# Kernel optimization log

Measured on AMD Instinct MI355X. Metric: run time of the kernel, lower is better.

## Reference

```python
import jax, jax.numpy as jnp
import numpy as np

# Fixed multi-scale geometry implied by the module's hard-coded reshapes
# (48^2=2304, 24^2=576, 12^2=144; Len_q = 576).
SPATIAL = [(48, 48), (24, 24), (12, 12)]
NH, NP, NL = 6, 4, 3  # num_heads, num_points, num_levels


def _process_reference_points(rp):
    """rp: (B, 3024, 2) normalized refs over 3 levels -> (B, 576, 2).
    Mirrors the part1/part2/part3 averaging in MSDeformAttn.forward."""
    B = rp.shape[0]
    p1 = rp[:, :2304].reshape(B, 48, 48, 2).mean(axis=(1, 2))[:, None, :]
    p1 = jnp.broadcast_to(p1, (B, 576, 2))
    p2 = rp[:, 2304:2880].reshape(B, 576, 2)
    p3 = rp[:, 2880:].reshape(B, 12, 12, 2)
    p3 = jax.image.resize(p3, (B, 24, 24, 2), 'bilinear')  # align_corners=False
    p3 = p3.reshape(B, 576, 2)
    return (p1 + p2 + p3) / 3.0


def _bilinear_sample(val_l, coords, Hl, Wl):
    """val_l: (B, Hl*Wl, nh, d) one level's values.
    coords: (B, Lq, nh, P, 2) normalized (x, y) sampling locations.
    Returns (B, Lq, P, nh, d) bilinearly sampled values (zero padding)."""
    B, Lq, nh, P, _ = coords.shape
    px = coords[..., 0] * Wl - 0.5
    py = coords[..., 1] * Hl - 0.5
    x0 = jnp.floor(px)
    y0 = jnp.floor(py)
    lx = px - x0
    ly = py - y0
    x0i = x0.astype(jnp.int32)
    y0i = y0.astype(jnp.int32)

    def _flat(a):  # (B,Lq,nh,P) -> (B,Lq*P,nh,1) matching value layout
        return a.transpose(0, 1, 3, 2).reshape(B, Lq * P, nh, 1)

    def gather(xi, yi):
        valid = (xi >= 0) & (xi < Wl) & (yi >= 0) & (yi < Hl)
        xi_c = jnp.clip(xi, 0, Wl - 1)
        yi_c = jnp.clip(yi, 0, Hl - 1)
        idx = _flat(yi_c * Wl + xi_c)
        v = jnp.take_along_axis(val_l, idx, axis=1)  # (B,Lq*P,nh,d)
        return v * _flat(valid).astype(val_l.dtype)

    w00 = _flat((1 - lx) * (1 - ly))
    w10 = _flat(lx * (1 - ly))
    w01 = _flat((1 - lx) * ly)
    w11 = _flat(lx * ly)
    out = (gather(x0i, y0i) * w00 + gather(x0i + 1, y0i) * w10 +
           gather(x0i, y0i + 1) * w01 + gather(x0i + 1, y0i + 1) * w11)
    return out.reshape(B, Lq, P, nh, -1)


def setup_inputs() -> dict:
    key = jax.random.key(0)
    ks = jax.random.split(key, 8)
    B, C = 32, 384
    Lq, Lv = 576, 3024
    # reference points exactly as get_reference_points builds them
    refs = []
    for (Hl, Wl) in SPATIAL:
        ry, rx = np.meshgrid(np.linspace(0.5, Hl - 0.5, Hl) / Hl,
                             np.linspace(0.5, Wl - 0.5, Wl) / Wl, indexing='ij')
        refs.append(np.stack([rx.ravel(), ry.ravel()], -1))
    rp = np.concatenate(refs, 0).astype(np.float32)  # (3024, 2)
    rp = np.broadcast_to(rp[None, :, None, :], (B, Lv, 1, 2)).copy()
    s = 1.0 / np.sqrt(C)
    return {
        'query': jax.random.normal(ks[0], (B, Lq, C), jnp.float32),
        'value': jax.random.normal(ks[1], (B, Lv, C), jnp.float32),
        'reference_points': jnp.asarray(rp),
        'W_value': jax.random.normal(ks[2], (C, C), jnp.float32) * s,
        'b_value': jnp.zeros((C,), jnp.float32),
        'W_off': jax.random.normal(ks[3], (C, NH * NL * NP * 2), jnp.float32) * 0.01,
        'b_off': jnp.zeros((NH * NL * NP * 2,), jnp.float32),
        'W_attn': jax.random.normal(ks[4], (C, NH * NL * NP), jnp.float32) * s,
        'b_attn': jnp.zeros((NH * NL * NP,), jnp.float32),
        'W_out': jax.random.normal(ks[5], (C, C), jnp.float32) * s,
        'b_out': jnp.zeros((C,), jnp.float32),
    }


def reference(query, value, reference_points, W_value, b_value, W_off, b_off,
              W_attn, b_attn, W_out, b_out):
    B, Lq, C = query.shape
    d = C // NH
    val = (value @ W_value + b_value).reshape(B, -1, NH, d)
    off = (query @ W_off + b_off).reshape(B, Lq, NH, NL, NP, 2)
    attn = jax.nn.softmax((query @ W_attn + b_attn)
                          .reshape(B, Lq, NH, NL * NP), axis=-1)
    attn = attn.reshape(B, Lq, NH, NL, NP)
    ref = _process_reference_points(reference_points.reshape(B, -1, 2))
    coords = off + ref[:, :, None, None, None, :]  # (B,Lq,nh,L,P,2)
    out = jnp.zeros((B, Lq, NH, d), query.dtype)
    start = 0
    for l, (Hl, Wl) in enumerate(SPATIAL):
        val_l = val[:, start:start + Hl * Wl]
        sampled = _bilinear_sample(val_l, coords[:, :, :, l], Hl, Wl)
        out = out + jnp.einsum('bqpnd,bqnp->bqnd', sampled, attn[:, :, :, l])
        start += Hl * Wl
    return out.reshape(B, Lq, NH * d) @ W_out + b_out
```

## Files before the change

kernel.cpp:

```cpp
#include <hip/hip_runtime.h>
#include <cmath>

#define B_SZ   32
#define LQ     576
#define LV     3024
#define CDIM   384
#define NHEAD  6
#define DHEAD  64
#define NLVL   3
#define NPTS   4
#define NPROJ  216
#define NPROJP 256

typedef short    bx4 __attribute__((ext_vector_type(4)));
typedef short    bx8 __attribute__((ext_vector_type(8)));
typedef float    fx4 __attribute__((ext_vector_type(4)));
typedef _Float16 hx8 __attribute__((ext_vector_type(8)));

__device__ __forceinline__ short f2bf(float f) {
    unsigned u = __builtin_bit_cast(unsigned, f);
    unsigned r = (u + 0x7FFFu + ((u >> 16) & 1u)) >> 16;
    return (short)r;
}
__device__ __forceinline__ float bf2f(unsigned short u) {
    return __builtin_bit_cast(float, ((unsigned)u) << 16);
}
__device__ __forceinline__ short f2h(float f) {
    return __builtin_bit_cast(short, (_Float16)f);
}

__global__ __launch_bounds__(256) void cast_transpose_kernel(
    const float* __restrict__ W, short* __restrict__ Wt, int K, int N)
{
    int idx = blockIdx.x * 256 + threadIdx.x;
    if (idx >= K * N) return;
    int n = idx / K, k = idx - n * K;
    Wt[idx] = f2bf(W[(size_t)k * N + n]);
}

__global__ __launch_bounds__(256) void prep_proj_f16_kernel(
    const float* __restrict__ W_off, const float* __restrict__ b_off,
    const float* __restrict__ W_attn, const float* __restrict__ b_attn,
    short* __restrict__ Wf, float* __restrict__ bc)
{
    int idx = blockIdx.x * 256 + threadIdx.x;
    if (idx >= NPROJP * CDIM) return;
    int n = idx / CDIM, k = idx - n * CDIM;
    float w = 0.f;
    if (n < 144)           w = W_off[(size_t)k * 144 + n];
    else if (n < NPROJ)    w = W_attn[(size_t)k * 72 + (n - 144)];
    Wf[idx] = f2h(w);
    if (idx < NPROJP)
        bc[idx] = (idx < 144) ? b_off[idx]
                 : (idx < NPROJ ? b_attn[idx - 144] : 0.f);
}

__global__ __launch_bounds__(512) void value_gemm_kernel(
    const float* __restrict__ A, const short* __restrict__ Bt,
    const float* __restrict__ bias, short* __restrict__ Cout,
    int M, int K)
{
    constexpr int N = 384;
    __shared__ short As[128 * 64];
    __shared__ short Bs[384 * 64];

    const int tid = threadIdx.x;
    const int m0 = blockIdx.x * 128;

    const int w  = tid >> 6;
    const int l  = tid & 63;
    const int wr = (w & 1) * 64;
    const int wc = (w >> 1) * 96;
    const int lr = l & 15;
    const int q  = l >> 4;

    const int rg  = l >> 3;
    const int cg  = l & 7;
    const int csw = cg ^ rg;

    const int am = tid >> 2;
    const int ak = (tid & 3) << 4;

    fx4 acc[4][6] = {};

    for (int k0 = 0; k0 < K; k0 += 64) {
        #pragma unroll
        for (int t = 0; t < 6; ++t) {
            const int rbase = w * 48 + t * 8;
            const short* gB = Bt + (size_t)(rbase + rg) * K + k0 + csw * 8;
            __builtin_amdgcn_global_load_lds(
                (const __attribute__((address_space(1))) void*)gB,
                (__attribute__((address_space(3))) void*)&Bs[rbase * 64],
                16, 0, 0);
        }
        {
            const float* gA = A + (size_t)(m0 + am) * K + k0 + ak;
            const float4 v0 = *(const float4*)(gA + 0);
            const float4 v1 = *(const float4*)(gA + 4);
            const float4 v2 = *(const float4*)(gA + 8);
            const float4 v3 = *(const float4*)(gA + 12);
            bx8 s0, s1;
            s0[0] = f2bf(v0.x); s0[1] = f2bf(v0.y); s0[2] = f2bf(v0.z); s0[3] = f2bf(v0.w);
            s0[4] = f2bf(v1.x); s0[5] = f2bf(v1.y); s0[6] = f2bf(v1.z); s0[7] = f2bf(v1.w);
            s1[0] = f2bf(v2.x); s1[1] = f2bf(v2.y); s1[2] = f2bf(v2.z); s1[3] = f2bf(v2.w);
            s1[4] = f2bf(v3.x); s1[5] = f2bf(v3.y); s1[6] = f2bf(v3.z); s1[7] = f2bf(v3.w);
            const int ob = ak >> 3;
            const int o0 = (ob + 0) ^ (am & 7);
            const int o1 = (ob + 1) ^ (am & 7);
            *(bx8*)&As[am * 64 + o0 * 8] = s0;
            *(bx8*)&As[am * 64 + o1 * 8] = s1;
        }
        __syncthreads();

        #pragma unroll
        for (int ks = 0; ks < 2; ++ks) {
            bx8 af[4], bf[6];
            #pragma unroll
            for (int i = 0; i < 4; ++i)
                af[i] = *(const bx8*)&As[(wr + i * 16 + lr) * 64 +
                                         (((ks * 4 + q) ^ (lr & 7)) << 3)];
            #pragma unroll
            for (int j = 0; j < 6; ++j)
                bf[j] = *(const bx8*)&Bs[(wc + j * 16 + lr) * 64 +
                                         (((ks * 4 + q) ^ (lr & 7)) << 3)];
            #pragma unroll
            for (int i = 0; i < 4; ++i)
                #pragma unroll
                for (int j = 0; j < 6; ++j)
                    acc[i][j] = __builtin_amdgcn_mfma_f32_16x16x32_bf16(
                        af[i], bf[j], acc[i][j], 0, 0, 0);
        }
        __syncthreads();
    }

    const int rrow = q * 4;
    #pragma unroll
    for (int j = 0; j < 6; ++j) {
        const int col = wc + j * 16 + lr;
        const float bv = bias[col];
        #pragma unroll
        for (int i = 0; i < 4; ++i) {
            const int row = m0 + wr + i * 16 + rrow;
            #pragma unroll
            for (int r = 0; r < 4; ++r)
                Cout[(size_t)(row + r) * N + col] = f2bf(acc[i][j][r] + bv);
        }
    }
}

template <bool OUT_BF16>
__global__ __launch_bounds__(256) void gemm_dma_kernel(
    const short* __restrict__ A, const short* __restrict__ Bt,
    const float* __restrict__ bias, void* __restrict__ Cout,
    int M, int K)
{
    constexpr int N = 384;
    __shared__ short As[128 * 64];
    __shared__ short Bs[128 * 64];

    const int tid = threadIdx.x;
    const int n0 = blockIdx.x * 128;
    const int m0 = blockIdx.y * 128;

    const int w  = tid >> 6;
    const int l  = tid & 63;
    const int wr = (w & 1) * 64;
    const int wc = (w >> 1) * 64;
    const int lr = l & 15;
    const int q  = l >> 4;

    const int rg  = l >> 3;
    const int cg  = l & 7;
    const int csw = cg ^ rg;

    fx4 acc[4][4] = {};

    for (int k0 = 0; k0 < K; k0 += 64) {
        #pragma unroll
        for (int t = 0; t < 4; ++t) {
            const int rbase = w * 32 + t * 8;
            const short* gA = A + (size_t)(m0 + rbase + rg) * K + k0 + csw * 8;
            __builtin_amdgcn_global_load_lds(
                (const __attribute__((address_space(1))) void*)gA,
                (__attribute__((address_space(3))) void*)&As[rbase * 64],
                16, 0, 0);
            const short* gB = Bt + (size_t)(n0 + rbase + rg) * K + k0 + csw * 8;
            __builtin_amdgcn_global_load_lds(
                (const __attribute__((address_space(1))) void*)gB,
                (__attribute__((address_space(3))) void*)&Bs[rbase * 64],
                16, 0, 0);
        }
        __syncthreads();

        #pragma unroll
        for (int ks = 0; ks < 2; ++ks) {
            bx8 af[4], bf[4];
            #pragma unroll
            for (int i = 0; i < 4; ++i)
                af[i] = *(const bx8*)&As[(wr + i * 16 + lr) * 64 +
                                         (((ks * 4 + q) ^ (lr & 7)) << 3)];
            #pragma unroll
            for (int j = 0; j < 4; ++j)
                bf[j] = *(const bx8*)&Bs[(wc + j * 16 + lr) * 64 +
                                         (((ks * 4 + q) ^ (lr & 7)) << 3)];
            #pragma unroll
            for (int i = 0; i < 4; ++i)
                #pragma unroll
                for (int j = 0; j < 4; ++j)
                    acc[i][j] = __builtin_amdgcn_mfma_f32_16x16x32_bf16(
                        af[i], bf[j], acc[i][j], 0, 0, 0);
        }
        __syncthreads();
    }

    const int rrow = q * 4;
    #pragma unroll
    for (int j = 0; j < 4; ++j) {
        const int col = n0 + wc + j * 16 + lr;
        const float bv = bias[col];
        #pragma unroll
        for (int i = 0; i < 4; ++i) {
            const int row = m0 + wr + i * 16 + rrow;
            #pragma unroll
            for (int r = 0; r < 4; ++r) {
                if (OUT_BF16)
                    ((short*)Cout)[(size_t)(row + r) * N + col] = f2bf(acc[i][j][r] + bv);
                else
                    ((float*)Cout)[(size_t)(row + r) * N + col] = acc[i][j][r] + bv;
            }
        }
    }
}

__global__ __launch_bounds__(256) void gemm_proj_kernel(
    const float* __restrict__ A, const short* __restrict__ Wf,
    const float* __restrict__ bias, float* __restrict__ C,
    int M, int K)
{
    __shared__ short As[128 * 72];
    __shared__ short Bs[128 * 72];

    const int tid = threadIdx.x;
    const int n0 = blockIdx.x * 128;
    const int m0 = blockIdx.y * 128;

    const int w  = tid >> 6;
    const int l  = tid & 63;
    const int wr = (w & 1) * 64;
    const int wc = (w >> 1) * 64;
    const int lr = l & 15;
    const int ko = (l >> 4) * 8;

    fx4 acc[4][4] = {};

    for (int k0 = 0; k0 < K; k0 += 64) {
        #pragma unroll
        for (int r = 0; r < 8; ++r) {
            const int id = tid + r * 256;
            const int m  = id >> 4;
            const int kq = (id & 15) << 2;
            const float4 v = *(const float4*)(A + (size_t)(m0 + m) * K + k0 + kq);
            bx4 s;
            s[0] = f2h(v.x); s[1] = f2h(v.y); s[2] = f2h(v.z); s[3] = f2h(v.w);
            *(bx4*)&As[m * 72 + kq] = s;
        }
        #pragma unroll
        for (int r = 0; r < 4; ++r) {
            const int id = tid + r * 256;
            const int n  = id >> 3;
            const int k8 = (id & 7) << 3;
            *(bx8*)&Bs[n * 72 + k8] = *(const bx8*)(Wf + (size_t)(n0 + n) * K + k0 + k8);
        }
        __syncthreads();

        #pragma unroll
        for (int ks = 0; ks < 2; ++ks) {
            bx8 af[4], bf[4];
            #pragma unroll
            for (int i = 0; i < 4; ++i)
                af[i] = *(const bx8*)&As[(wr + i * 16 + lr) * 72 + ks * 32 + ko];
            #pragma unroll
            for (int j = 0; j < 4; ++j)
                bf[j] = *(const bx8*)&Bs[(wc + j * 16 + lr) * 72 + ks * 32 + ko];
            #pragma unroll
            for (int i = 0; i < 4; ++i)
                #pragma unroll
                for (int j = 0; j < 4; ++j)
                    acc[i][j] = __builtin_amdgcn_mfma_f32_16x16x32_f16(
                        __builtin_bit_cast(hx8, af[i]),
                        __builtin_bit_cast(hx8, bf[j]), acc[i][j], 0, 0, 0);
        }
        __syncthreads();
    }

    const int rrow = (l >> 4) * 4;
    #pragma unroll
    for (int j = 0; j < 4; ++j) {
        const int col = n0 + wc + j * 16 + lr;
        if (col >= NPROJ) continue;
        const float bv = bias[col];
        #pragma unroll
        for (int i = 0; i < 4; ++i) {
            const int row = m0 + wr + i * 16 + rrow;
            #pragma unroll
            for (int r = 0; r < 4; ++r)
                C[(size_t)(row + r) * NPROJ + col] = acc[i][j][r] + bv;
        }
    }
}

__global__ __launch_bounds__(256) void ref_kernel(
    const float* __restrict__ rp, float* __restrict__ refp)
{
    const int b = blockIdx.x;
    const float* r = rp + (size_t)b * LV * 2;
    const int tid = threadIdx.x;

    __shared__ float redx[256], redy[256];
    float sx = 0.f, sy = 0.f;
    for (int i = tid; i < 2304; i += 256) {
        sx += r[2 * i + 0];
        sy += r[2 * i + 1];
    }
    redx[tid] = sx; redy[tid] = sy;
    __syncthreads();
    for (int s = 128; s > 0; s >>= 1) {
        if (tid < s) { redx[tid] += redx[tid + s]; redy[tid] += redy[tid + s]; }
        __syncthreads();
    }
    const float p1x = redx[0] * (1.f / 2304.f);
    const float p1y = redy[0] * (1.f / 2304.f);

    const float* g = r + 2880 * 2;
    for (int q = tid; q < 576; q += 256) {
        const float p2x = r[(2304 + q) * 2 + 0];
        const float p2y = r[(2304 + q) * 2 + 1];
        const int qy = q / 24, qx = q % 24;
        const float syc = fminf(fmaxf(0.5f * qy - 0.25f, 0.f), 11.f);
        const float sxc = fminf(fmaxf(0.5f * qx - 0.25f, 0.f), 11.f);
        int y0 = min((int)syc, 10);
        int x0 = min((int)sxc, 10);
        const float fy = syc - (float)y0, fx = sxc - (float)x0;
        const float v00x = g[(y0 * 12 + x0) * 2 + 0],     v00y = g[(y0 * 12 + x0) * 2 + 1];
        const float v10x = g[(y0 * 12 + x0 + 1) * 2 + 0], v10y = g[(y0 * 12 + x0 + 1) * 2 + 1];
        const float v01x = g[((y0 + 1) * 12 + x0) * 2 + 0],     v01y = g[((y0 + 1) * 12 + x0) * 2 + 1];
        const float v11x = g[((y0 + 1) * 12 + x0 + 1) * 2 + 0], v11y = g[((y0 + 1) * 12 + x0 + 1) * 2 + 1];
        const float p3x = (1.f - fy) * ((1.f - fx) * v00x + fx * v10x)
                        + fy * ((1.f - fx) * v01x + fx * v11x);
        const float p3y = (1.f - fy) * ((1.f - fx) * v00y + fx * v10y)
                        + fy * ((1.f - fx) * v01y + fx * v11y);
        refp[((size_t)b * LQ + q) * 2 + 0] = (p1x + p2x + p3x) * (1.f / 3.f);
        refp[((size_t)b * LQ + q) * 2 + 1] = (p1y + p2y + p3y) * (1.f / 3.f);
    }
}

__global__ __launch_bounds__(192) void sample_kernel(
    const unsigned short* __restrict__ val, const float* __restrict__ proj,
    const float* __restrict__ refp, unsigned* __restrict__ mid)
{
    const int i = blockIdx.x;
    const int g = i & 7;
    const int r = i >> 3;
    const int b = g * 4 + (r / LQ);
    const int q = r - (r / LQ) * LQ;
    const int bq = b * LQ + q;
    const int tid = threadIdx.x;

    __shared__ float attn[72];
    __shared__ int   sloc[72][4];
    __shared__ float swt[72][4];

    if (tid < 72) {
        attn[tid] = proj[(size_t)bq * NPROJ + 144 + tid];

        const int h = tid / 12;
        const int rr = tid % 12;
        const int l = rr >> 2;
        const int p = rr & 3;

        const int HL[3] = {48, 24, 12};
        const int ST[3] = {0, 2304, 2880};
        const int Hl = HL[l], Wl = HL[l], st = ST[l];

        const float rx = refp[bq * 2 + 0];
        const float ry = refp[bq * 2 + 1];
        const int oc = ((h * NLVL + l) * NPTS + p) * 2;
        const float cx = proj[(size_t)bq * NPROJ + oc + 0] + rx;
        const float cy = proj[(size_t)bq * NPROJ + oc + 1] + ry;

        const float px = cx * (float)Wl - 0.5f;
        const float py = cy * (float)Hl - 0.5f;
        const float x0f = floorf(px), y0f = floorf(py);
        const float lx = px - x0f, ly = py - y0f;
        const int x0 = (int)x0f, y0 = (int)y0f;

        #pragma unroll
        for (int k = 0; k < 4; ++k) {
            const int dx = k & 1, dy = k >> 1;
            const int xi = x0 + dx, yi = y0 + dy;
            const bool v = (xi >= 0) && (xi < Wl) && (yi >= 0) && (yi < Hl);
            const int xc = min(max(xi, 0), Wl - 1);
            const int yc = min(max(yi, 0), Hl - 1);
            sloc[tid][k] = st + yc * Wl + xc;
            const float wx = dx ? lx : 1.f - lx;
            const float wy = dy ? ly : 1.f - ly;
            swt[tid][k] = v ? wx * wy : 0.f;
        }
    }
    __syncthreads();

    if (tid < NHEAD) {
        float mx = -1e30f;
        #pragma unroll
        for (int j = 0; j < 12; ++j) mx = fmaxf(mx, attn[tid * 12 + j]);
        float s = 0.f;
        #pragma unroll
        for (int j = 0; j < 12; ++j) {
            const float e = expf(attn[tid * 12 + j] - mx);
            attn[tid * 12 + j] = e;
            s += e;
        }
        const float inv = 1.f / s;
        #pragma unroll
        for (int j = 0; j < 12; ++j) attn[tid * 12 + j] *= inv;
    }
    __syncthreads();

    const int h  = tid >> 5;
    const int c2 = (tid & 31) << 1;
    const unsigned* vp = (const unsigned*)(val + (size_t)b * LV * CDIM + h * DHEAD + c2);
    float acc0 = 0.f, acc1 = 0.f;
    #pragma unroll
    for (int s = 0; s < 12; ++s) {
        const int j = h * 12 + s;
        const float a = attn[j];
        float s0 = 0.f, s1 = 0.f;
        #pragma unroll
        for (int k = 0; k < 4; ++k) {
            const unsigned u = vp[(size_t)sloc[j][k] * (CDIM / 2)];
            const float lo = __builtin_bit_cast(float, u << 16);
            const float hi = __builtin_bit_cast(float, u & 0xFFFF0000u);
            s0 += swt[j][k] * lo;
            s1 += swt[j][k] * hi;
        }
        acc0 += a * s0;
        acc1 += a * s1;
    }
    const unsigned lo = (unsigned)(unsigned short)f2bf(acc0);
    const unsigned hi = (unsigned)(unsigned short)f2bf(acc1);
    mid[((size_t)bq * CDIM + h * DHEAD + c2) >> 1] = lo | (hi << 16);
}

extern "C" void kernel_launch(void* const* d_in, const int* in_sizes, int n_in,
                              void* d_out, int out_size, void* d_ws, size_t ws_size,
                              hipStream_t stream)
{
    (void)in_sizes; (void)n_in; (void)out_size; (void)ws_size;

    const float* query   = (const float*)d_in[0];
    const float* value   = (const float*)d_in[1];
    const float* rp      = (const float*)d_in[2];
    const float* W_value = (const float*)d_in[3];
    const float* b_value = (const float*)d_in[4];
    const float* W_off   = (const float*)d_in[5];
    const float* b_off   = (const float*)d_in[6];
    const float* W_attn  = (const float*)d_in[7];
    const float* b_attn  = (const float*)d_in[8];
    const float* W_out   = (const float*)d_in[9];
    const float* b_out   = (const float*)d_in[10];
    float* out = (float*)d_out;

    char* p = (char*)d_ws;
    auto take = [&](size_t bytes) { char* q = p; p += (bytes + 255) & ~(size_t)255; return q; };
    short* val  = (short*)take((size_t)B_SZ * LV * CDIM * 2);
    short* mid  = (short*)take((size_t)B_SZ * LQ * CDIM * 2);
    short* Wtv  = (short*)take((size_t)CDIM * CDIM * 2);
    short* Wto  = (short*)take((size_t)CDIM * CDIM * 2);
    short* Wf   = (short*)take((size_t)NPROJP * CDIM * 2);
    float* proj = (float*)take((size_t)B_SZ * LQ * NPROJ * 4);
    float* refp = (float*)take((size_t)B_SZ * LQ * 2 * 4);
    float* bc   = (float*)take((size_t)NPROJP * 4);

    const int Mv = B_SZ * LV;
    const int Mq = B_SZ * LQ;

    cast_transpose_kernel<<<(CDIM * CDIM + 255) / 256, 256, 0, stream>>>(
        W_value, Wtv, CDIM, CDIM);
    cast_transpose_kernel<<<(CDIM * CDIM + 255) / 256, 256, 0, stream>>>(
        W_out, Wto, CDIM, CDIM);
    prep_proj_f16_kernel<<<(NPROJP * CDIM + 255) / 256, 256, 0, stream>>>(
        W_off, b_off, W_attn, b_attn, Wf, bc);

    value_gemm_kernel<<<Mv / 128, 512, 0, stream>>>(
        value, Wtv, b_value, val, Mv, CDIM);
    gemm_proj_kernel<<<dim3(2, Mq / 128), 256, 0, stream>>>(
        query, Wf, bc, proj, Mq, CDIM);
    ref_kernel<<<B_SZ, 256, 0, stream>>>(rp, refp);
    sample_kernel<<<Mq, 192, 0, stream>>>(
        (const unsigned short*)val, proj, refp, (unsigned*)mid);
    gemm_dma_kernel<false><<<dim3(3, Mq / 128), 256, 0, stream>>>(
        mid, Wto, b_out, out, Mq, CDIM);
}
```

Measured before the change: 368.3 us.

## Double-buffer value GEMM B tiles and prefetch A into registers

Restructures the value projection GEMM main loop into a software pipeline. The next K-slice of the B matrix is loaded asynchronously into a second LDS buffer and the next A slice is held in registers while the current tile's MFMAs run. The aim is to hide global memory latency behind compute. In exchange, the B shared buffer doubles to 96KB and register pressure rises, which may reduce occupancy. The loop also hard-codes NK=6, so it assumes K=384.

```diff
diff --git a/kernel.cpp b/kernel.cpp
--- a/kernel.cpp
+++ b/kernel.cpp
@@ -61,8 +61,9 @@
     int M, int K)
 {
     constexpr int N = 384;
+    constexpr int NK = 6;
     __shared__ short As[128 * 64];
-    __shared__ short Bs[384 * 64];
+    __shared__ short Bs[2 * 384 * 64];
 
     const int tid = threadIdx.x;
     const int m0 = blockIdx.x * 128;
@@ -80,57 +81,92 @@
 
     const int am = tid >> 2;
     const int ak = (tid & 3) << 4;
+    const float* gA = A + (size_t)(m0 + am) * K + ak;
+    const int ob = ak >> 3;
+    const int o0 = (ob + 0) ^ (am & 7);
+    const int o1 = (ob + 1) ^ (am & 7);
 
     fx4 acc[4][6] = {};
 
-    for (int k0 = 0; k0 < K; k0 += 64) {
-        #pragma unroll
-        for (int t = 0; t < 6; ++t) {
-            const int rbase = w * 48 + t * 8;
-            const short* gB = Bt + (size_t)(rbase + rg) * K + k0 + csw * 8;
-            __builtin_amdgcn_global_load_lds(
-                (const __attribute__((address_space(1))) void*)gB,
-                (__attribute__((address_space(3))) void*)&Bs[rbase * 64],
-                16, 0, 0);
-        }
-        {
-            const float* gA = A + (size_t)(m0 + am) * K + k0 + ak;
-            const float4 v0 = *(const float4*)(gA + 0);
-            const float4 v1 = *(const float4*)(gA + 4);
-            const float4 v2 = *(const float4*)(gA + 8);
-            const float4 v3 = *(const float4*)(gA + 12);
+    #pragma unroll
+    for (int t = 0; t < 6; ++t) {
+        const int rbase = w * 48 + t * 8;
+        const short* gB = Bt + (size_t)(rbase + rg) * K + csw * 8;
+        __builtin_amdgcn_global_load_lds(
+            (const __attribute__((address_space(1))) void*)gB,
+            (__attribute__((address_space(3))) void*)&Bs[rbase * 64],
+            16, 0, 0);
+    }
+    float4 v0 = *(const float4*)(gA + 0);
+    float4 v1 = *(const float4*)(gA + 4);
+    float4 v2 = *(const float4*)(gA + 8);
+    float4 v3 = *(const float4*)(gA + 12);
+    {
+        bx8 s0, s1;
+        s0[0] = f2bf(v0.x); s0[1] = f2bf(v0.y); s0[2] = f2bf(v0.z); s0[3] = f2bf(v0.w);
+        s0[4] = f2bf(v1.x); s0[5] = f2bf(v1.y); s0[6] = f2bf(v1.z); s0[7] = f2bf(v1.w);
+        s1[0] = f2bf(v2.x); s1[1] = f2bf(v2.y); s1[2] = f2bf(v2.z); s1[3] = f2bf(v2.w);
+        s1[4] = f2bf(v3.x); s1[5] = f2bf(v3.y); s1[6] = f2bf(v3.z); s1[7] = f2bf(v3.w);
+        *(bx8*)&As[am * 64 + o0 * 8] = s0;
+        *(bx8*)&As[am * 64 + o1 * 8] = s1;
+    }
+    __syncthreads();
+
+    #pragma unroll
+    for (int t = 0; t < NK; ++t) {
+        const int cur = t & 1;
+
+        if (t + 1 < NK) {
+            const int nxt = (t + 1) & 1;
+            #pragma unroll
+            for (int u = 0; u < 6; ++u) {
+                const int rbase = w * 48 + u * 8;
+                const short* gB = Bt + (size_t)(rbase + rg) * K
+                                     + (t + 1) * 64 + csw * 8;
+                __builtin_amdgcn_global_load_lds(
+                    (const __attribute__((address_space(1))) void*)gB,
+                    (__attribute__((address_space(3))) void*)
+                        &Bs[nxt * 384 * 64 + rbase * 64],
+                    16, 0, 0);
+            }
+            const float* gAt = gA + (t + 1) * 64;
+            v0 = *(const float4*)(gAt + 0);
+            v1 = *(const float4*)(gAt + 4);
+            v2 = *(const float4*)(gAt + 8);
+            v3 = *(const float4*)(gAt + 12);
+        }
+
+        #pragma unroll
+        for (int ks = 0; ks < 2; ++ks) {
+            bx8 af[4], bf[6];
+            #pragma unroll
+            for (int i = 0; i < 4; ++i)
+                af[i] = *(const bx8*)&As[(wr + i * 16 + lr) * 64 +
+                                         (((ks * 4 + q) ^ (lr & 7)) << 3)];
+            #pragma unroll
+            for (int j = 0; j < 6; ++j)
+                bf[j] = *(const bx8*)&Bs[cur * 384 * 64 +
+                                         (wc + j * 16 + lr) * 64 +
+                                         (((ks * 4 + q) ^ (lr & 7)) << 3)];
+            #pragma unroll
+            for (int i = 0; i < 4; ++i)
+                #pragma unroll
+                for (int j = 0; j < 6; ++j)
+                    acc[i][j] = __builtin_amdgcn_mfma_f32_16x16x32_bf16(
+                        af[i], bf[j], acc[i][j], 0, 0, 0);
+        }
+        __syncthreads();
+
+        if (t + 1 < NK) {
             bx8 s0, s1;
             s0[0] = f2bf(v0.x); s0[1] = f2bf(v0.y); s0[2] = f2bf(v0.z); s0[3] = f2bf(v0.w);
             s0[4] = f2bf(v1.x); s0[5] = f2bf(v1.y); s0[6] = f2bf(v1.z); s0[7] = f2bf(v1.w);
             s1[0] = f2bf(v2.x); s1[1] = f2bf(v2.y); s1[2] = f2bf(v2.z); s1[3] = f2bf(v2.w);
             s1[4] = f2bf(v3.x); s1[5] = f2bf(v3.y); s1[6] = f2bf(v3.z); s1[7] = f2bf(v3.w);
-            const int ob = ak >> 3;
-            const int o0 = (ob + 0) ^ (am & 7);
-            const int o1 = (ob + 1) ^ (am & 7);
             *(bx8*)&As[am * 64 + o0 * 8] = s0;
             *(bx8*)&As[am * 64 + o1 * 8] = s1;
-        }
-        __syncthreads();
-
-        #pragma unroll
-        for (int ks = 0; ks < 2; ++ks) {
-            bx8 af[4], bf[6];
-            #pragma unroll
-            for (int i = 0; i < 4; ++i)
-                af[i] = *(const bx8*)&As[(wr + i * 16 + lr) * 64 +
-                                         (((ks * 4 + q) ^ (lr & 7)) << 3)];
-            #pragma unroll
-            for (int j = 0; j < 6; ++j)
-                bf[j] = *(const bx8*)&Bs[(wc + j * 16 + lr) * 64 +
-                                         (((ks * 4 + q) ^ (lr & 7)) << 3)];
-            #pragma unroll
-            for (int i = 0; i < 4; ++i)
-                #pragma unroll
-                for (int j = 0; j < 6; ++j)
-                    acc[i][j] = __builtin_amdgcn_mfma_f32_16x16x32_bf16(
-                        af[i], bf[j], acc[i][j], 0, 0, 0);
-        }
-        __syncthreads();
+            __syncthreads();
+        }
     }
 
     const int rrow = q * 4;
```

After: 370.8 us. No clear change (+0.7%).
